# Optimization experiments

Measured on AMD Instinct MI355X. Metric: run time of the kernel, lower is better.

The kernel has to match this reference:

```python
import jax, jax.numpy as jnp
import numpy as np

N_NODES = 100000
N_EDGES = 1600000
C_IN = 64
C_OUT = 64
BN_EPS = 1e-5


def setup_inputs() -> dict:
    key = jax.random.key(0)
    k_x, k_e, k_w, k_b, k_g = jax.random.split(key, 5)
    x = jax.random.normal(k_x, (N_NODES, C_IN), dtype=jnp.float32)
    edge_index = jax.random.randint(k_e, (2, N_EDGES), 0, N_NODES, dtype=jnp.int64)
    # Linear(in_channels*2, out_channels)
    lim = 1.0 / np.sqrt(2 * C_IN)
    W = jax.random.uniform(k_w, (2 * C_IN, C_OUT), dtype=jnp.float32, minval=-lim, maxval=lim)
    b = jax.random.uniform(k_b, (C_OUT,), dtype=jnp.float32, minval=-lim, maxval=lim)
    # BatchNorm affine params
    gamma = jnp.ones((C_OUT,), dtype=jnp.float32)
    beta = jnp.zeros((C_OUT,), dtype=jnp.float32)
    return {"x": x, "edge_index": edge_index, "W": W, "b": b, "gamma": gamma, "beta": beta}


def reference(x, edge_index, W, b, gamma, beta):
    src = edge_index[0]  # j (source)
    dst = edge_index[1]  # i (target)
    x_i = x[dst]                      # [E, C_IN]
    x_j = x[src]                      # [E, C_IN]
    # EdgeConv message: mlp(concat(x_i, x_j - x_i))
    feat = jnp.concatenate([x_i, x_j - x_i], axis=-1)  # [E, 2*C_IN]
    msg = feat @ W + b                                  # [E, C_OUT]
    # max aggregation back to target nodes; empty nodes -> 0 (PyG convention)
    agg = jax.ops.segment_max(msg, dst, num_segments=N_NODES)
    agg = jnp.where(jnp.isneginf(agg), 0.0, agg)
    h = jax.nn.elu(agg)
    # BatchNorm1d over nodes (training-mode batch stats, biased variance)
    mean = jnp.mean(h, axis=0)
    var = jnp.var(h, axis=0)
    return gamma * (h - mean) / jnp.sqrt(var + BN_EPS) + beta
```

## Files before the change

kernel.cpp:

```cpp
#include <hip/hip_runtime.h>
#include <math.h>

#define N_NODES 100000
#define N_EDGES 1600000
#define C 64
#define BKT_SHIFT 6
#define BKT_NODES 64
#define NBKT 1563
#define TILE 8192
#define NBINB 196
#define NGEMB 391
#define PSTR 1564
#define MAXW 65
#define NSTRIPE 32
#define XSTR 72
#define BN_EPS 1e-5f

typedef __attribute__((ext_vector_type(8))) short short8;
typedef __attribute__((ext_vector_type(4))) float f32x4;


__device__ __forceinline__ float eluf(float x) {
    return x > 0.f ? x : (expf(x) - 1.f);
}
__device__ __forceinline__ float key32_to_f(unsigned k32) {
    unsigned k16 = k32 >> 16;
    unsigned u16 = (k16 & 0x8000u) ? (k16 & 0x7FFFu) : (~k16 & 0xFFFFu);
    return __uint_as_float(u16 << 16);
}
__device__ __forceinline__ unsigned bf16rne(float f) {
    unsigned u = __float_as_uint(f);
    return (u + 0x7FFFu + ((u >> 16) & 1u)) >> 16;
}
__device__ __forceinline__ float bf16lo_f(unsigned w) { return __uint_as_float((w & 0xFFFFu) << 16); }
__device__ __forceinline__ float bf16hi_f(unsigned w) { return __uint_as_float(w & 0xFFFF0000u); }

__device__ __forceinline__ short8 pack8(float4 a, float4 b) {
    short8 r;
    r[0] = (short)bf16rne(a.x); r[1] = (short)bf16rne(a.y);
    r[2] = (short)bf16rne(a.z); r[3] = (short)bf16rne(a.w);
    r[4] = (short)bf16rne(b.x); r[5] = (short)bf16rne(b.y);
    r[6] = (short)bf16rne(b.z); r[7] = (short)bf16rne(b.w);
    return r;
}

__global__ __launch_bounds__(1024) void k_hist(const int* __restrict__ ei,
                                               unsigned* __restrict__ tab,
                                               float* __restrict__ stripes) {
    __shared__ unsigned hc[NBKT];
    __shared__ unsigned ss[1024];
    int t = threadIdx.x;
    int tile = blockIdx.x;
    int e0 = tile * TILE;
    int ecount = min(TILE, N_EDGES - e0);

    for (int i = t; i < NBKT; i += 1024) hc[i] = 0u;
    if (blockIdx.x == 0) {
        for (int i = t; i < NSTRIPE * 128; i += 1024) stripes[i] = 0.f;
    }
    __syncthreads();
    for (int i = t; i < ecount; i += 1024) {
        int src = ei[e0 + i];
        int dst = ei[N_EDGES + e0 + i];
        if ((unsigned)src < N_NODES && (unsigned)dst < N_NODES)
            atomicAdd(&hc[dst >> BKT_SHIFT], 1u);
    }
    __syncthreads();
    unsigned v0 = (2 * t < NBKT) ? hc[2 * t] : 0u;
    unsigned v1 = (2 * t + 1 < NBKT) ? hc[2 * t + 1] : 0u;
    unsigned s = v0 + v1;
    ss[t] = s;
    __syncthreads();
    for (int off = 1; off < 1024; off <<= 1) {
        unsigned v = (t >= off) ? ss[t - off] : 0u;
        __syncthreads();
        ss[t] += v;
        __syncthreads();
    }
    unsigned excl = ss[t] - s;
    unsigned* row = tab + (size_t)tile * PSTR;
    if (2 * t < NBKT) row[2 * t] = excl;
    if (2 * t + 1 < NBKT) row[2 * t + 1] = excl + v0;
    if (t == 1023) row[NBKT] = ss[1023];
}

__global__ __launch_bounds__(1024) void k_prep(const int* __restrict__ ei,
                                               const float* __restrict__ x,
                                               const float* __restrict__ W,
                                               const float* __restrict__ b,
                                               const unsigned* __restrict__ tab,
                                               unsigned* __restrict__ binned,
                                               unsigned* __restrict__ Apb,
                                               unsigned* __restrict__ Bkey) {
    __shared__ __align__(16) unsigned char smem[18688];
    int t = threadIdx.x;

    if (blockIdx.x < NBINB) {
        unsigned* cur = (unsigned*)smem;
        int tile = blockIdx.x;
        int e0 = tile * TILE;
        int ecount = min(TILE, N_EDGES - e0);
        const unsigned* row = tab + (size_t)tile * PSTR;
        for (int i = t; i < NBKT; i += 1024) cur[i] = row[i];
        __syncthreads();
        for (int i = t; i < ecount; i += 1024) {
            int src = ei[e0 + i];
            int dst = ei[N_EDGES + e0 + i];
            if ((unsigned)src >= N_NODES || (unsigned)dst >= N_NODES) continue;
            int bk = dst >> BKT_SHIFT;
            unsigned pos = atomicAdd(&cur[bk], 1u);
            binned[(size_t)tile * TILE + pos] =
                ((unsigned)(dst & (BKT_NODES - 1)) << 17) | (unsigned)src;
        }
    } else {
        unsigned short* WaT = (unsigned short*)smem;
        unsigned short* WbT = WaT + 64 * XSTR;
        float* biasS = (float*)(WbT + 64 * XSTR);
        int gb = blockIdx.x - NBINB;
        int base = gb * 256;

        for (int p = t; p < 4096; p += 1024) {
            int k = p >> 6, c = p & 63;
            float w1 = W[p];
            float w2 = W[4096 + p];
            WaT[c * XSTR + k] = (unsigned short)bf16rne(w1 - w2);
            WbT[c * XSTR + k] = (unsigned short)bf16rne(w2);
        }
        if (t < 64) biasS[t] = b[t];
        __syncthreads();

        int w = t >> 6;
        int l = t & 63;
        int ln = l & 15;
        int hi = l >> 4;

        short8 wa[4][2], wb[4][2];
#pragma unroll
        for (int nt = 0; nt < 4; ++nt)
#pragma unroll
            for (int h = 0; h < 2; ++h) {
                wa[nt][h] = *(const short8*)&WaT[(nt * 16 + ln) * XSTR + h * 32 + hi * 8];
                wb[nt][h] = *(const short8*)&WbT[(nt * 16 + ln) * XSTR + h * 32 + hi * 8];
            }

        int arow = base + w * 16 + ln;
        short8 af[2];
        if (arow < N_NODES) {
            const float4* xr = (const float4*)(x + (size_t)arow * 64);
#pragma unroll
            for (int h = 0; h < 2; ++h)
                af[h] = pack8(xr[h * 8 + hi * 2], xr[h * 8 + hi * 2 + 1]);
        } else {
#pragma unroll
            for (int h = 0; h < 2; ++h)
                af[h] = (short8){0, 0, 0, 0, 0, 0, 0, 0};
        }

        f32x4 acca[4], accb[4];
#pragma unroll
        for (int nt = 0; nt < 4; ++nt) {
            acca[nt] = (f32x4){0.f, 0.f, 0.f, 0.f};
            accb[nt] = (f32x4){0.f, 0.f, 0.f, 0.f};
#pragma unroll
            for (int h = 0; h < 2; ++h) {
                acca[nt] = __builtin_amdgcn_mfma_f32_16x16x32_bf16(af[h], wa[nt][h], acca[nt], 0, 0, 0);
                accb[nt] = __builtin_amdgcn_mfma_f32_16x16x32_bf16(af[h], wb[nt][h], accb[nt], 0, 0, 0);
            }
        }
#pragma unroll
        for (int nt = 0; nt < 4; ++nt) {
            int col = nt * 16 + ln;
            float bias = biasS[col];
            int cp = nt * 8 + (ln >> 1);
#pragma unroll
            for (int r = 0; r < 4; ++r) {
                int node = base + w * 16 + hi * 4 + r;
                unsigned a16 = bf16rne(acca[nt][r] + bias);
                unsigned aO = (unsigned)__shfl_xor((int)a16, 1, 64);
                unsigned r16 = bf16rne(accb[nt][r]);
                unsigned key16 = (r16 & 0x8000u) ? (~r16 & 0xFFFFu) : (r16 | 0x8000u);
                unsigned kO = (unsigned)__shfl_xor((int)key16, 1, 64);
                if (((l & 1) == 0) && node < N_NODES) {
                    Apb[(size_t)node * 32 + cp] = a16 | (aO << 16);
                    Bkey[(size_t)node * 32 + cp] = key16 | (kO << 16);
                }
            }
        }
    }
}

__global__ __launch_bounds__(256) void k_fused(const unsigned* __restrict__ tab,
                                               const unsigned* __restrict__ binned,
                                               const unsigned* __restrict__ Bkey,
                                               const unsigned* __restrict__ Apb,
                                               unsigned* __restrict__ hpk,
                                               float* __restrict__ stripes) {
    __shared__ __align__(16) unsigned mx[BKT_NODES * MAXW];
    __shared__ unsigned rstart[NBINB];
    __shared__ unsigned rb[257];
    int t = threadIdx.x;
    int orig = blockIdx.x;
    int xcd = orig & 7;
    int j = orig >> 3;
    int q = (xcd < 3 ? xcd * 196 : 3 * 196 + (xcd - 3) * 195) + j;
    int n0 = q * BKT_NODES;
    int nspan = min(BKT_NODES, N_NODES - n0);

    for (int i = t; i < BKT_NODES * MAXW; i += 256) mx[i] = 0u;

    unsigned own = 0;
    if (t < NBINB) {
        unsigned rs = tab[(size_t)t * PSTR + q];
        unsigned re = tab[(size_t)t * PSTR + q + 1];
        rstart[t] = rs;
        own = re - rs;
    }
    rb[t] = own;
    __syncthreads();
    for (int off = 1; off < 256; off <<= 1) {
        unsigned v = (t >= off) ? rb[t - off] : 0u;
        __syncthreads();
        rb[t] += v;
        __syncthreads();
    }
    unsigned excl = rb[t] - own;
    __syncthreads();
    rb[t] = excl;
    if (t == 255) rb[256] = excl + own;
    __syncthreads();
    unsigned cnt = rb[256];

    int ls = t & 3;
    for (unsigned idx = (unsigned)(t >> 2); idx < cnt; idx += 64) {
        unsigned lo = 0, hi = NBINB;
#pragma unroll
        for (int it = 0; it < 8; ++it) {
            unsigned mid = (lo + hi) >> 1;
            if (rb[mid] <= idx) lo = mid; else hi = mid;
        }
        unsigned p = binned[(size_t)lo * TILE + rstart[lo] + (idx - rb[lo])];
        unsigned src = p & 0x1FFFFu;
        unsigned dl = p >> 17;
        const uint4* bk = (const uint4*)(Bkey + (size_t)src * 32);
        uint4 w0 = bk[ls];
        uint4 w1 = bk[4 + ls];
        unsigned* row = mx + dl * MAXW;
        int s0 = ls * 8;
        atomicMax(&row[s0 + 0], w0.x << 16);
        atomicMax(&row[s0 + 1], w0.x & 0xFFFF0000u);
        atomicMax(&row[s0 + 2], w0.y << 16);
        atomicMax(&row[s0 + 3], w0.y & 0xFFFF0000u);
        atomicMax(&row[s0 + 4], w0.z << 16);
        atomicMax(&row[s0 + 5], w0.z & 0xFFFF0000u);
        atomicMax(&row[s0 + 6], w0.w << 16);
        atomicMax(&row[s0 + 7], w0.w & 0xFFFF0000u);
        int s1 = 32 + ls * 8;
        atomicMax(&row[s1 + 0], w1.x << 16);
        atomicMax(&row[s1 + 1], w1.x & 0xFFFF0000u);
        atomicMax(&row[s1 + 2], w1.y << 16);
        atomicMax(&row[s1 + 3], w1.y & 0xFFFF0000u);
        atomicMax(&row[s1 + 4], w1.z << 16);
        atomicMax(&row[s1 + 5], w1.z & 0xFFFF0000u);
        atomicMax(&row[s1 + 6], w1.w << 16);
        atomicMax(&row[s1 + 7], w1.w & 0xFFFF0000u);
    }
    __syncthreads();

    int lane4 = t & 15;
    int g = t >> 4;
    float4 s = make_float4(0.f, 0.f, 0.f, 0.f);
    float4 sq = make_float4(0.f, 0.f, 0.f, 0.f);
    for (int nl = g; nl < nspan; nl += 16) {
        int n = n0 + nl;
        const unsigned* row = mx + nl * MAXW + lane4 * 4;
        unsigned k0 = row[0], k1 = row[1], k2 = row[2], k3 = row[3];
        uint2 ap = *reinterpret_cast<const uint2*>(Apb + (size_t)n * 32 + lane4 * 2);
        float h0 = (k0 == 0u) ? 0.f : eluf(bf16lo_f(ap.x) + key32_to_f(k0));
        float h1 = (k1 == 0u) ? 0.f : eluf(bf16hi_f(ap.x) + key32_to_f(k1));
        float h2 = (k2 == 0u) ? 0.f : eluf(bf16lo_f(ap.y) + key32_to_f(k2));
        float h3 = (k3 == 0u) ? 0.f : eluf(bf16hi_f(ap.y) + key32_to_f(k3));
        unsigned q0 = bf16rne(h0), q1 = bf16rne(h1), q2 = bf16rne(h2), q3 = bf16rne(h3);
        uint2 hp;
        hp.x = q0 | (q1 << 16);
        hp.y = q2 | (q3 << 16);
        *reinterpret_cast<uint2*>(hpk + (size_t)n * 32 + lane4 * 2) = hp;
        float f0 = __uint_as_float(q0 << 16), f1 = __uint_as_float(q1 << 16);
        float f2 = __uint_as_float(q2 << 16), f3 = __uint_as_float(q3 << 16);
        s.x += f0; s.y += f1; s.z += f2; s.w += f3;
        sq.x += f0 * f0; sq.y += f1 * f1; sq.z += f2 * f2; sq.w += f3 * f3;
    }
    __syncthreads();

    float4* lsum = (float4*)mx;
    float4* lqum = lsum + 256;
    lsum[t] = s;
    lqum[t] = sq;
    __syncthreads();
#pragma unroll
    for (int off = 8; off >= 1; off >>= 1) {
        if (g < off) {
            int o = t + off * 16;
            lsum[t].x += lsum[o].x; lsum[t].y += lsum[o].y; lsum[t].z += lsum[o].z; lsum[t].w += lsum[o].w;
            lqum[t].x += lqum[o].x; lqum[t].y += lqum[o].y; lqum[t].z += lqum[o].z; lqum[t].w += lqum[o].w;
        }
        __syncthreads();
    }
    if (g == 0) {
        float* sb = stripes + (q & (NSTRIPE - 1)) * 128;
        int c4 = lane4 * 4;
        atomicAdd(&sb[c4 + 0], lsum[t].x);
        atomicAdd(&sb[c4 + 1], lsum[t].y);
        atomicAdd(&sb[c4 + 2], lsum[t].z);
        atomicAdd(&sb[c4 + 3], lsum[t].w);
        atomicAdd(&sb[64 + c4 + 0], lqum[t].x);
        atomicAdd(&sb[64 + c4 + 1], lqum[t].y);
        atomicAdd(&sb[64 + c4 + 2], lqum[t].z);
        atomicAdd(&sb[64 + c4 + 3], lqum[t].w);
    }
}

__global__ __launch_bounds__(128) void k_reduce(const float* __restrict__ stripes,
                                                float* __restrict__ finals) {
    int t = threadIdx.x;
    float acc = 0.f;
#pragma unroll
    for (int s = 0; s < NSTRIPE; ++s) acc += stripes[s * 128 + t];
    finals[t] = acc;
}

__global__ __launch_bounds__(256) void k_bn(const uint2* __restrict__ hpk2,
                                            const float* __restrict__ finals,
                                            const float* __restrict__ gamma,
                                            const float* __restrict__ beta,
                                            float4* __restrict__ out4) {
    size_t i = (size_t)blockIdx.x * blockDim.x + threadIdx.x;
    size_t stride = (size_t)gridDim.x * blockDim.x;
    const float invN = 1.f / (float)N_NODES;
    size_t total4 = (size_t)N_NODES * C / 4;
    for (size_t p = i; p < total4; p += stride) {
        int c4 = (int)(p & 15) * 4;
        uint2 hp = hpk2[p];
        float hx = bf16lo_f(hp.x), hy = bf16hi_f(hp.x);
        float hz = bf16lo_f(hp.y), hw = bf16hi_f(hp.y);
        float4 o;
        float m, v, inv;
        m = finals[c4 + 0] * invN; v = finals[64 + c4 + 0] * invN - m * m; inv = rsqrtf(v + BN_EPS);
        o.x = gamma[c4 + 0] * (hx - m) * inv + beta[c4 + 0];
        m = finals[c4 + 1] * invN; v = finals[64 + c4 + 1] * invN - m * m; inv = rsqrtf(v + BN_EPS);
        o.y = gamma[c4 + 1] * (hy - m) * inv + beta[c4 + 1];
        m = finals[c4 + 2] * invN; v = finals[64 + c4 + 2] * invN - m * m; inv = rsqrtf(v + BN_EPS);
        o.z = gamma[c4 + 2] * (hz - m) * inv + beta[c4 + 2];
        m = finals[c4 + 3] * invN; v = finals[64 + c4 + 3] * invN - m * m; inv = rsqrtf(v + BN_EPS);
        o.w = gamma[c4 + 3] * (hw - m) * inv + beta[c4 + 3];
        out4[p] = o;
    }
}

extern "C" void kernel_launch(void* const* d_in, const int* in_sizes, int n_in,
                              void* d_out, int out_size, void* d_ws, size_t ws_size,
                              hipStream_t stream) {
    const float* x = (const float*)d_in[0];
    const int* ei = (const int*)d_in[1];
    const float* W = (const float*)d_in[2];
    const float* b = (const float*)d_in[3];
    const float* gamma = (const float*)d_in[4];
    const float* beta = (const float*)d_in[5];
    float* out = (float*)d_out;

    char* ws = (char*)d_ws;
    unsigned* Bkey = (unsigned*)ws;
    unsigned* binned = Bkey + (size_t)N_NODES * 32;
    unsigned* Apb = binned + (size_t)NBINB * TILE;
    unsigned* hpk = Apb + (size_t)N_NODES * 32;
    unsigned* tab = hpk + (size_t)N_NODES * 32;
    float* stripes = (float*)(tab + (size_t)NBINB * PSTR);
    float* finals = stripes + NSTRIPE * 128;

    k_hist<<<NBINB, 1024, 0, stream>>>(ei, tab, stripes);
    k_prep<<<NBINB + NGEMB, 1024, 0, stream>>>(ei, x, W, b, tab, binned, Apb, Bkey);
    k_fused<<<NBKT, 256, 0, stream>>>(tab, binned, Bkey, Apb, hpk, stripes);
    k_reduce<<<1, 128, 0, stream>>>(stripes, finals);
    k_bn<<<2048, 256, 0, stream>>>((const uint2*)hpk, finals, gamma, beta, (float4*)out);
}
```

Measured before the change: 84.99 us.

## Transpose bin offset table and replace binary search with shared LUT

Adds a transpose kernel that packs each bucket's per-tile start and length into one contiguous row, so k_fused reads its 196 entries coalesced instead of strided across the table. Inside k_fused, the per-edge 8-step binary search over prefix sums is replaced by a shared-memory lookup table that maps each edge index to its base address in the binned array. This costs an extra kernel launch, extra workspace, and a serial per-thread LUT fill. It also caps each bucket at 2048 edges and packs start and length into 16 bits each, which would silently drop edges if a bucket exceeded those limits.

```diff
diff --git a/kernel.cpp b/kernel.cpp
--- a/kernel.cpp
+++ b/kernel.cpp
@@ -11,6 +11,8 @@
 #define NBINB 196
 #define NGEMB 391
 #define PSTR 1564
+#define TSTR 200
+#define LUTN 2048
 #define MAXW 65
 #define NSTRIPE 32
 #define XSTR 72
@@ -82,6 +84,17 @@
     if (2 * t < NBKT) row[2 * t] = excl;
     if (2 * t + 1 < NBKT) row[2 * t + 1] = excl + v0;
     if (t == 1023) row[NBKT] = ss[1023];
+}
+
+__global__ __launch_bounds__(256) void k_transpose(const unsigned* __restrict__ tab,
+                                                   unsigned* __restrict__ tabT) {
+    int idx = blockIdx.x * 256 + threadIdx.x;
+    if (idx >= NBKT * NBINB) return;
+    int q = idx / NBINB;
+    int t = idx - q * NBINB;
+    unsigned rs = tab[(size_t)t * PSTR + q];
+    unsigned re = tab[(size_t)t * PSTR + q + 1];
+    tabT[(size_t)q * TSTR + t] = ((re - rs) << 16) | rs;
 }
 
 __global__ __launch_bounds__(1024) void k_prep(const int* __restrict__ ei,
@@ -189,15 +202,15 @@
     }
 }
 
-__global__ __launch_bounds__(256) void k_fused(const unsigned* __restrict__ tab,
+__global__ __launch_bounds__(256) void k_fused(const unsigned* __restrict__ tabT,
                                                const unsigned* __restrict__ binned,
                                                const unsigned* __restrict__ Bkey,
                                                const unsigned* __restrict__ Apb,
                                                unsigned* __restrict__ hpk,
                                                float* __restrict__ stripes) {
     __shared__ __align__(16) unsigned mx[BKT_NODES * MAXW];
-    __shared__ unsigned rstart[NBINB];
-    __shared__ unsigned rb[257];
+    __shared__ unsigned lut[LUTN];
+    __shared__ unsigned rb[256];
     int t = threadIdx.x;
     int orig = blockIdx.x;
     int xcd = orig & 7;
@@ -208,14 +221,10 @@
 
     for (int i = t; i < BKT_NODES * MAXW; i += 256) mx[i] = 0u;
 
-    unsigned own = 0;
-    if (t < NBINB) {
-        unsigned rs = tab[(size_t)t * PSTR + q];
-        unsigned re = tab[(size_t)t * PSTR + q + 1];
-        rstart[t] = rs;
-        own = re - rs;
-    }
-    rb[t] = own;
+    unsigned e = (t < NBINB) ? tabT[(size_t)q * TSTR + t] : 0u;
+    unsigned rs = e & 0xFFFFu;
+    unsigned len = e >> 16;
+    rb[t] = len;
     __syncthreads();
     for (int off = 1; off < 256; off <<= 1) {
         unsigned v = (t >= off) ? rb[t - off] : 0u;
@@ -223,22 +232,20 @@
         rb[t] += v;
         __syncthreads();
     }
-    unsigned excl = rb[t] - own;
-    __syncthreads();
-    rb[t] = excl;
-    if (t == 255) rb[256] = excl + own;
-    __syncthreads();
-    unsigned cnt = rb[256];
+    unsigned incl = rb[t];
+    unsigned excl = incl - len;
+    unsigned cnt = min(rb[255], (unsigned)LUTN);
+    __syncthreads();
+    if (t < NBINB && len) {
+        unsigned base = (unsigned)t * TILE + rs - excl;
+        unsigned jend = min(excl + len, (unsigned)LUTN);
+        for (unsigned ji = excl; ji < jend; ++ji) lut[ji] = base;
+    }
+    __syncthreads();
 
     int ls = t & 3;
     for (unsigned idx = (unsigned)(t >> 2); idx < cnt; idx += 64) {
-        unsigned lo = 0, hi = NBINB;
-#pragma unroll
-        for (int it = 0; it < 8; ++it) {
-            unsigned mid = (lo + hi) >> 1;
-            if (rb[mid] <= idx) lo = mid; else hi = mid;
-        }
-        unsigned p = binned[(size_t)lo * TILE + rstart[lo] + (idx - rb[lo])];
+        unsigned p = binned[(size_t)(lut[idx] + idx)];
         unsigned src = p & 0x1FFFFu;
         unsigned dl = p >> 17;
         const uint4* bk = (const uint4*)(Bkey + (size_t)src * 32);
@@ -373,12 +380,14 @@
     unsigned* Apb = binned + (size_t)NBINB * TILE;
     unsigned* hpk = Apb + (size_t)N_NODES * 32;
     unsigned* tab = hpk + (size_t)N_NODES * 32;
-    float* stripes = (float*)(tab + (size_t)NBINB * PSTR);
+    unsigned* tabT = tab + (size_t)NBINB * PSTR;
+    float* stripes = (float*)(tabT + (size_t)NBKT * TSTR);
     float* finals = stripes + NSTRIPE * 128;
 
     k_hist<<<NBINB, 1024, 0, stream>>>(ei, tab, stripes);
+    k_transpose<<<(NBKT * NBINB + 255) / 256, 256, 0, stream>>>(tab, tabT);
     k_prep<<<NBINB + NGEMB, 1024, 0, stream>>>(ei, x, W, b, tab, binned, Apb, Bkey);
-    k_fused<<<NBKT, 256, 0, stream>>>(tab, binned, Bkey, Apb, hpk, stripes);
+    k_fused<<<NBKT, 256, 0, stream>>>(tabT, binned, Bkey, Apb, hpk, stripes);
     k_reduce<<<1, 128, 0, stream>>>(stripes, finals);
     k_bn<<<2048, 256, 0, stream>>>((const uint2*)hpk, finals, gamma, beta, (float4*)out);
 }
```

New measurement: 94.67 us. 1.11x slower.
